# Kernel optimization log

Hardware: AMD Instinct MI355X
Metric: run time of the kernel (lower is better)

Reference implementation:

```python
import jax, jax.numpy as jnp
import numpy as np

N, E, B = 50000, 400000, 50
F_IN, HID, HEADS, F_OUT = 128, 32, 8, 64
HC = HID * HEADS  # 256


def gat_conv(x, src, dst, W, a_s, a_d, b, n):
    """PyG-style GATConv (concat=True, negative_slope=0.2), inference mode."""
    H, C = a_s.shape
    h = (x @ W).reshape(n, H, C)                       # [N,H,C]
    alpha_s = (h * a_s).sum(-1)                        # [N,H]
    alpha_d = (h * a_d).sum(-1)                        # [N,H]
    logits = jax.nn.leaky_relu(alpha_s[src] + alpha_d[dst], 0.2)  # [E,H]
    m = jax.ops.segment_max(logits, dst, num_segments=n)
    m = jnp.where(jnp.isfinite(m), m, 0.0)
    e = jnp.exp(logits - m[dst])
    den = jax.ops.segment_sum(e, dst, num_segments=n)
    alpha = e / (den[dst] + 1e-16)                     # segment softmax over dst
    out = jax.ops.segment_sum(h[src] * alpha[:, :, None], dst, num_segments=n)
    return out.reshape(n, H * C) + b


def setup_inputs() -> dict:
    key = jax.random.key(0)
    ks = jax.random.split(key, 24)
    s = 0.1
    inp = {
        "x": jax.random.normal(ks[0], (N, F_IN), jnp.float32),
        "edge_index": jax.random.randint(ks[1], (2, E), 0, N),
        "batch": jnp.sort(jax.random.randint(ks[2], (N,), 0, B)),
        "W1": jax.random.normal(ks[3], (F_IN, HC), jnp.float32) * s,
        "a_src1": jax.random.normal(ks[4], (HEADS, HID), jnp.float32) * s,
        "a_dst1": jax.random.normal(ks[5], (HEADS, HID), jnp.float32) * s,
        "b1": jnp.zeros((HC,), jnp.float32),
        "W2": jax.random.normal(ks[6], (HC, HC), jnp.float32) * s,
        "a_src2": jax.random.normal(ks[7], (1, HC), jnp.float32) * s,
        "a_dst2": jax.random.normal(ks[8], (1, HC), jnp.float32) * s,
        "b2": jnp.zeros((HC,), jnp.float32),
        "W3": jax.random.normal(ks[9], (HC, HC), jnp.float32) * s,
        "a_src3": jax.random.normal(ks[10], (1, HC), jnp.float32) * s,
        "a_dst3": jax.random.normal(ks[11], (1, HC), jnp.float32) * s,
        "b3": jnp.zeros((HC,), jnp.float32),
        "W4": jax.random.normal(ks[12], (HC, F_OUT), jnp.float32) * s,
        "a_src4": jax.random.normal(ks[13], (1, F_OUT), jnp.float32) * s,
        "a_dst4": jax.random.normal(ks[14], (1, F_OUT), jnp.float32) * s,
        "b4": jnp.zeros((F_OUT,), jnp.float32),
        "Wl": jax.random.normal(ks[15], (F_OUT, 1), jnp.float32) * s,
        "bl": jnp.zeros((1,), jnp.float32),
    }
    return inp


def reference(x, edge_index, batch, W1, a_src1, a_dst1, b1, W2, a_src2, a_dst2, b2,
              W3, a_src3, a_dst3, b3, W4, a_src4, a_dst4, b4, Wl, bl):
    n = x.shape[0]
    loop = jnp.arange(n)
    src = jnp.concatenate([edge_index[0], loop])  # add self loops (PyG default)
    dst = jnp.concatenate([edge_index[1], loop])
    x = jax.nn.elu(gat_conv(x, src, dst, W1, a_src1, a_dst1, b1, n))
    x = jax.nn.elu(gat_conv(x, src, dst, W2, a_src2, a_dst2, b2, n))
    x = jax.nn.elu(gat_conv(x, src, dst, W3, a_src3, a_dst3, b3, n))
    x_gat = gat_conv(x, src, dst, W4, a_src4, a_dst4, b4, n)
    # to_dense_batch(x_gat, batch).mean(dim=1): sum per graph / max graph size
    counts = jax.ops.segment_sum(jnp.ones((n,), x_gat.dtype), batch, num_segments=B)
    max_nodes = counts.max()
    pooled = jax.ops.segment_sum(x_gat, batch, num_segments=B) / max_nodes  # [B,F_OUT]
    return pooled @ Wl + bl  # [B,1]
```

## Files before the change

kernel.cpp:

```cpp
#include <hip/hip_runtime.h>
#include <math.h>


typedef __attribute__((ext_vector_type(8))) short short8;
typedef __attribute__((ext_vector_type(4))) float f32x4;

__device__ __forceinline__ unsigned short f2bf(float f) {
  unsigned int u = __builtin_bit_cast(unsigned int, f);
  unsigned int r = u + 0x7FFFu + ((u >> 16) & 1u);
  return (unsigned short)(r >> 16);
}
__device__ __forceinline__ float bf2f(unsigned short h) {
  unsigned int u = ((unsigned int)h) << 16;
  return __builtin_bit_cast(float, u);
}
__device__ __forceinline__ unsigned short f2h(float f) {
  _Float16 h = (_Float16)f;
  return __builtin_bit_cast(unsigned short, h);
}
__device__ __forceinline__ float h2f(unsigned short u) {
  return (float)__builtin_bit_cast(_Float16, u);
}

__device__ __forceinline__ void gload16(const unsigned short* g, unsigned short* l) {
  __builtin_amdgcn_global_load_lds(
      (const __attribute__((address_space(1))) void*)g,
      (__attribute__((address_space(3))) void*)l, 16, 0, 0);
}

template<int H>
__global__ __launch_bounds__(256) void k_gemm_mfma(
    const unsigned short* __restrict__ A2, const unsigned short* __restrict__ Wt,
    unsigned short* __restrict__ C, const float* __restrict__ avec_s,
    const float* __restrict__ avec_d, float* __restrict__ outS,
    float* __restrict__ outD, int M, int Kb, int Nc)
{
  __shared__ unsigned short lds[12288];
  unsigned short* As = lds;
  unsigned short* Bs = lds + 4096;
  const int tid = threadIdx.x;
  const int w = tid >> 6, l = tid & 63;
  const int row0 = blockIdx.x * 64, col0 = blockIdx.y * 128;
  const int wr = w >> 1, wc = w & 1;
  const int fr = l & 15, kg = l >> 4;
  const int xr = (fr & 7) << 4;
  const int sK = 2 * Kb;
  const int csrc = 8 * ((l & 7) ^ ((l >> 3) & 7));
  const int lrow = l >> 3;

  f32x4 acc[2][4];
  #pragma unroll
  for (int i = 0; i < 2; i++)
    #pragma unroll
    for (int j = 0; j < 4; j++) acc[i][j] = (f32x4){0.f, 0.f, 0.f, 0.f};

  for (int kp = 0; kp < sK; kp += 64) {
    #pragma unroll
    for (int i = 0; i < 2; i++) {
      int q = w * 2 + i;
      gload16(&A2[(size_t)(row0 + q * 8 + lrow) * sK + (kp + csrc)], &As[q * 512]);
    }
    #pragma unroll
    for (int i = 0; i < 4; i++) {
      int q = w * 4 + i;
      gload16(&Wt[(size_t)(col0 + q * 8 + lrow) * sK + (kp + csrc)], &Bs[q * 512]);
    }
    __syncthreads();
    #pragma unroll
    for (int kk = 0; kk < 2; kk++) {
      short8 a[2], b[4];
      #pragma unroll
      for (int mi = 0; mi < 2; mi++) {
        int r = wr * 32 + mi * 16 + fr;
        int off = r * 128 + ((kk * 64 + kg * 16) ^ xr);
        a[mi] = *(const short8*)((const char*)As + off);
      }
      #pragma unroll
      for (int ni = 0; ni < 4; ni++) {
        int c = wc * 64 + ni * 16 + fr;
        int off = c * 128 + ((kk * 64 + kg * 16) ^ xr);
        b[ni] = *(const short8*)((const char*)Bs + off);
      }
      #pragma unroll
      for (int mi = 0; mi < 2; mi++)
        #pragma unroll
        for (int ni = 0; ni < 4; ni++)
          acc[mi][ni] = __builtin_amdgcn_mfma_f32_16x16x32_bf16(
              a[mi], b[ni], acc[mi][ni], 0, 0, 0);
    }
    __syncthreads();
  }

  #pragma unroll
  for (int mi = 0; mi < 2; mi++)
    #pragma unroll
    for (int ni = 0; ni < 4; ni++)
      #pragma unroll
      for (int rr = 0; rr < 4; rr++) {
        int row = wr * 32 + mi * 16 + kg * 4 + rr;
        int c = wc * 64 + ni * 16 + fr;
        int sc = c ^ (((row >> 1) & 7) << 3);
        lds[row * 128 + sc] = f2h(acc[mi][ni][rr]);
      }
  __syncthreads();

  constexpr int RW = (H == 8) ? 4 : 16;
  const int Ch = Nc / H;
  const int rbase = tid >> 4;
  const int cc = tid & 15;
  const int c0 = cc * 8;
  const int gc0 = col0 + c0;
  float as8[8], ad8[8];
  #pragma unroll
  for (int j = 0; j < 8; j++) {
    bool ok = (gc0 + j) < Nc;
    as8[j] = ok ? avec_s[gc0 + j] : 0.f;
    ad8[j] = ok ? avec_d[gc0 + j] : 0.f;
  }
  #pragma unroll
  for (int i = 0; i < 4; i++) {
    int row = rbase + i * 16;
    int gr = row0 + row;
    int scc = c0 ^ (((row >> 1) & 7) << 3);
    short8 cv = *(const short8*)&lds[row * 128 + scc];
    if (gr < M && gc0 < Nc)
      *(short8*)&C[(size_t)gr * Nc + gc0] = cv;
    float ps = 0.f, pd = 0.f;
    #pragma unroll
    for (int j = 0; j < 8; j++) {
      float cf = h2f((unsigned short)cv[j]);
      ps = fmaf(cf, as8[j], ps);
      pd = fmaf(cf, ad8[j], pd);
    }
    #pragma unroll
    for (int off = 1; off < RW; off <<= 1) {
      ps += __shfl_xor(ps, off);
      pd += __shfl_xor(pd, off);
    }
    if ((tid & (RW - 1)) == 0 && gr < M) {
      int head = gc0 / Ch;
      atomicAdd(&outS[gr * H + head], ps);
      atomicAdd(&outD[gr * H + head], pd);
    }
  }
}

__global__ __launch_bounds__(256) void k_packX(const float* __restrict__ x,
    unsigned short* __restrict__ A2, int N, int Mpad)
{
  int row = blockIdx.x * 8 + (threadIdx.x >> 5);
  int c = (threadIdx.x & 31) * 4;
  if (row >= Mpad) return;
  float4 v = make_float4(0.f, 0.f, 0.f, 0.f);
  if (row < N) v = *(const float4*)&x[(size_t)row * 128 + c];
  float f[4] = {v.x, v.y, v.z, v.w};
  unsigned short hi[4], lo[4];
  #pragma unroll
  for (int i = 0; i < 4; i++) {
    hi[i] = f2bf(f[i]);
    lo[i] = f2bf(f[i] - bf2f(hi[i]));
  }
  size_t base = (size_t)row * 256 + c;
  *(uint2*)&A2[base] = make_uint2((unsigned)hi[0] | ((unsigned)hi[1] << 16),
                                  (unsigned)hi[2] | ((unsigned)hi[3] << 16));
  *(uint2*)&A2[base + 128] = make_uint2((unsigned)lo[0] | ((unsigned)lo[1] << 16),
                                        (unsigned)lo[2] | ((unsigned)lo[3] << 16));
}

__global__ void k_packW(const float* __restrict__ W, unsigned short* __restrict__ Wt,
                        int K, int NC, int NCPAD)
{
  int idx = blockIdx.x * 256 + threadIdx.x;
  int K2 = 2 * K;
  if (idx >= NCPAD * K2) return;
  int c = idx / K2, kp = idx % K2;
  unsigned short o = 0;
  if (c < NC) o = f2bf(W[(size_t)(kp % K) * NC + c]);
  Wt[(size_t)c * K2 + kp] = o;
}

template<int H>
__global__ void k_wcomp(const float* __restrict__ aS, const float* __restrict__ aD,
    const int* __restrict__ col, const int* __restrict__ rid,
    float* __restrict__ wbuf, int M)
{
  int idx = blockIdx.x * 256 + threadIdx.x;
  if (idx >= M) return;
  int e = idx / H, hd = idx % H;
  int s = col[e], r = rid[e];
  float lg = aS[s * H + hd] + aD[r * H + hd];
  lg = fmaxf(lg, 0.2f * lg);
  wbuf[idx] = __expf(lg);
}

template<int H, int HC, int ELU, int SPLIT>
__global__ __launch_bounds__(256) void k_aggregate(const unsigned short* __restrict__ h,
    const float* __restrict__ wbuf,
    const int* __restrict__ rowptr, const int* __restrict__ col,
    const float* __restrict__ bias, float* __restrict__ xout,
    unsigned short* __restrict__ a2out, int N)
{
  constexpr int VEC = HC / 64;
  constexpr int C = HC / H;
  constexpr int CH = (H == 8) ? 8 : 64;
  __shared__ float wlds[4][64];
  int wave = threadIdx.x >> 6, lane = threadIdx.x & 63;
  int row = blockIdx.x * 4 + wave;
  if (row >= N) return;
  const int cb = lane * VEC;
  const int hdg = cb / C;
  int s0 = rowptr[row], s1 = rowptr[row + 1];

  float den = 0.f;
  float acc[VEC];
  #pragma unroll
  for (int v = 0; v < VEC; v++) acc[v] = 0.f;

  for (int base = s0; base < s1; base += CH) {
    int cnt = min(CH, s1 - base);
    int eo = (H == 8) ? (lane >> 3) : lane;
    bool valid = eo < cnt;
    int s = col[valid ? (base + eo) : (s1 - 1)];
    float wv = valid ? wbuf[(size_t)base * H + lane] : 0.f;
    float d = wv;
    if constexpr (H == 8) {
      d += __shfl_xor(d, 8); d += __shfl_xor(d, 16); d += __shfl_xor(d, 32);
      wlds[wave][lane] = wv;
    } else {
      #pragma unroll
      for (int off = 1; off < 64; off <<= 1) d += __shfl_xor(d, off);
    }
    den += d;
    if (H == 8) {
      asm volatile("s_waitcnt lgkmcnt(0)" ::: "memory");
    }
    #pragma unroll 2
    for (int j = 0; j < cnt; j++) {
      int sj = __builtin_amdgcn_readlane(s, (H == 8) ? (j * 8) : j);
      float wj;
      if constexpr (H == 8) {
        wj = wlds[wave][j * 8 + hdg];
      } else {
        wj = __builtin_bit_cast(float,
              __builtin_amdgcn_readlane(__builtin_bit_cast(int, wv), j));
      }
      if constexpr (VEC == 4) {
        uint2 raw = *(const uint2*)&h[(size_t)sj * HC + cb];
        acc[0] = fmaf(wj, h2f((unsigned short)(raw.x & 0xFFFF)), acc[0]);
        acc[1] = fmaf(wj, h2f((unsigned short)(raw.x >> 16)),    acc[1]);
        acc[2] = fmaf(wj, h2f((unsigned short)(raw.y & 0xFFFF)), acc[2]);
        acc[3] = fmaf(wj, h2f((unsigned short)(raw.y >> 16)),    acc[3]);
      } else {
        acc[0] = fmaf(wj, h2f(h[(size_t)sj * HC + cb]), acc[0]);
      }
    }
  }
  if (H == 8) den = __shfl(den, hdg);
  float inv = 1.f / (den + 1e-16f);
  float o[VEC];
  #pragma unroll
  for (int v = 0; v < VEC; v++) {
    float t = acc[v] * inv + bias[cb + v];
    if (ELU) t = t > 0.f ? t : expm1f(t);
    o[v] = t;
  }
  if constexpr (SPLIT) {
    unsigned short hi[4], lo[4];
    #pragma unroll
    for (int v = 0; v < 4; v++) {
      hi[v] = f2bf(o[v]);
      lo[v] = f2bf(o[v] - bf2f(hi[v]));
    }
    size_t b2 = (size_t)row * (2 * HC) + cb;
    *(uint2*)&a2out[b2] = make_uint2((unsigned)hi[0] | ((unsigned)hi[1] << 16),
                                     (unsigned)hi[2] | ((unsigned)hi[3] << 16));
    *(uint2*)&a2out[b2 + HC] = make_uint2((unsigned)lo[0] | ((unsigned)lo[1] << 16),
                                          (unsigned)lo[2] | ((unsigned)lo[3] << 16));
  } else if constexpr (VEC == 4) {
    *(float4*)&xout[(size_t)row * HC + cb] = make_float4(o[0], o[1], o[2], o[3]);
  } else {
    xout[(size_t)row * HC + cb] = o[0];
  }
}

__global__ void k_init(int* deg, float* pool, unsigned short* A2, int N, int B,
                       int Mpad) {
  int i = blockIdx.x * 256 + threadIdx.x;
  if (i < N) deg[i] = 1;
  if (i < B * 64) pool[i] = 0.f;
  int padn = (Mpad - N) * 512;
  if (i < padn) A2[(size_t)N * 512 + i] = 0;
}

__global__ void k_deg(const int* __restrict__ ei, int* deg, int E) {
  int e = blockIdx.x * 256 + threadIdx.x;
  if (e < E) atomicAdd(&deg[ei[E + e]], 1);
}

__global__ void k_counts(const int* __restrict__ bat, int* cnt, int N, int B) {
  int b = threadIdx.x;
  if (b >= B) return;
  int lo0 = 0, hi0 = N;
  while (lo0 < hi0) { int mid = (lo0 + hi0) >> 1; if (bat[mid] < b) lo0 = mid + 1; else hi0 = mid; }
  int lo1 = lo0, hi1 = N;
  while (lo1 < hi1) { int mid = (lo1 + hi1) >> 1; if (bat[mid] < b + 1) lo1 = mid + 1; else hi1 = mid; }
  cnt[b] = lo1 - lo0;
}

__global__ __launch_bounds__(256) void k_scan1(const int* __restrict__ deg,
                                               int* csum, int N, int chunk) {
  int bid = blockIdx.x, t = threadIdx.x;
  int lo = bid * chunk, hi = min(lo + chunk, N);
  int s = 0;
  for (int i = lo + t; i < hi; i += 256) s += deg[i];
  #pragma unroll
  for (int off = 32; off; off >>= 1) s += __shfl_xor(s, off);
  __shared__ int sh[4];
  if ((t & 63) == 0) sh[t >> 6] = s;
  __syncthreads();
  if (t == 0) csum[bid] = sh[0] + sh[1] + sh[2] + sh[3];
}

__global__ __launch_bounds__(256) void k_scan2(const int* __restrict__ csum,
                                               int* coff) {
  __shared__ int s[256];
  int t = threadIdx.x;
  int v0 = csum[t];
  s[t] = v0;
  for (int off = 1; off < 256; off <<= 1) {
    __syncthreads();
    int v = (t >= off) ? s[t - off] : 0;
    __syncthreads();
    s[t] += v;
  }
  __syncthreads();
  coff[t] = s[t] - v0;
}

__global__ __launch_bounds__(256) void k_scan3(const int* __restrict__ deg,
    const int* __restrict__ coff, int* rowptr, int* cursor, int N, int chunk) {
  __shared__ int s[256];
  int bid = blockIdx.x, t = threadIdx.x;
  int i = bid * chunk + t;
  int v = (t < chunk && i < N) ? deg[i] : 0;
  s[t] = v;
  for (int off = 1; off < 256; off <<= 1) {
    __syncthreads();
    int x = (t >= off) ? s[t - off] : 0;
    __syncthreads();
    s[t] += x;
  }
  __syncthreads();
  int excl = s[t] - v + coff[bid];
  if (t < chunk && i < N) {
    rowptr[i] = excl;
    cursor[i] = excl;
    if (i == N - 1) rowptr[N] = excl + v;
  }
}

__global__ void k_scatter(const int* __restrict__ ei, int* cursor, int* col,
                          int* rid, int E, int N) {
  int idx = blockIdx.x * 256 + threadIdx.x;
  if (idx >= E + N) return;
  int s, d;
  if (idx < E) { s = ei[idx]; d = ei[E + idx]; }
  else         { s = d = idx - E; }
  int pos = atomicAdd(&cursor[d], 1);
  col[pos] = s;
  rid[pos] = d;
}

__global__ __launch_bounds__(256) void k_pool(const float* __restrict__ xg,
    const int* __restrict__ bat, float* pool, int N) {
  int lane = threadIdx.x & 63, w = threadIdx.x >> 6;
  int base = (blockIdx.x * 4 + w) * 16;
  if (base >= N) return;
  int end = min(base + 16, N);
  float local = 0.f;
  int curb = bat[base];
  for (int n = base; n < end; n++) {
    int b = bat[n];
    if (b != curb) {
      atomicAdd(&pool[curb * 64 + lane], local);
      local = 0.f; curb = b;
    }
    local += xg[(size_t)n * 64 + lane];
  }
  atomicAdd(&pool[curb * 64 + lane], local);
}

__global__ void k_final(const float* __restrict__ pool, const int* __restrict__ cnt,
    const float* __restrict__ Wl, const float* __restrict__ bl,
    float* __restrict__ out, int B) {
  int lane = threadIdx.x;
  int c = (lane < B) ? cnt[lane] : 0;
  #pragma unroll
  for (int off = 32; off; off >>= 1) c = max(c, __shfl_xor(c, off));
  float invm = 1.f / (float)c;
  float wl = Wl[lane];
  for (int b = 0; b < B; b++) {
    float ps = pool[b * 64 + lane] * wl;
    #pragma unroll
    for (int off = 32; off; off >>= 1) ps += __shfl_xor(ps, off);
    if (lane == 0) out[b] = ps * invm + bl[0];
  }
}

extern "C" void kernel_launch(void* const* d_in, const int* in_sizes, int n_in,
                              void* d_out, int out_size, void* d_ws, size_t ws_size,
                              hipStream_t stream)
{
  (void)n_in; (void)ws_size;
  const float* x   = (const float*)d_in[0];
  const int*   ei  = (const int*)d_in[1];
  const int*   bat = (const int*)d_in[2];
  const float* W1  = (const float*)d_in[3];
  const float* as1 = (const float*)d_in[4];
  const float* ad1 = (const float*)d_in[5];
  const float* b1  = (const float*)d_in[6];
  const float* W2  = (const float*)d_in[7];
  const float* as2 = (const float*)d_in[8];
  const float* ad2 = (const float*)d_in[9];
  const float* b2  = (const float*)d_in[10];
  const float* W3  = (const float*)d_in[11];
  const float* as3 = (const float*)d_in[12];
  const float* ad3 = (const float*)d_in[13];
  const float* b3  = (const float*)d_in[14];
  const float* W4  = (const float*)d_in[15];
  const float* as4 = (const float*)d_in[16];
  const float* ad4 = (const float*)d_in[17];
  const float* b4  = (const float*)d_in[18];
  const float* Wl  = (const float*)d_in[19];
  const float* bl  = (const float*)d_in[20];
  float* out = (float*)d_out;

  const int N = in_sizes[0] / 128;
  const int E = in_sizes[1] / 2;
  const int B = out_size;
  const int Mpad = ((N + 127) / 128) * 128;
  const int EN = E + N;

  char* p = (char*)d_ws;
  auto alloc = [&](size_t bytes) -> void* {
    void* r = (void*)p;
    p += ((bytes + 255) & ~(size_t)255);
    return r;
  };
  unsigned short* A2 = (unsigned short*)alloc((size_t)Mpad * 512 * 2);
  unsigned short* hbuf = (unsigned short*)alloc((size_t)N * 256 * 2);
  unsigned short* w2t1 = (unsigned short*)alloc((size_t)256 * 512 * 2);
  unsigned short* w2t2 = (unsigned short*)alloc((size_t)256 * 512 * 2);
  unsigned short* w2t3 = (unsigned short*)alloc((size_t)256 * 512 * 2);
  unsigned short* w2t4 = (unsigned short*)alloc((size_t)128 * 512 * 2);
  float* aAll  = (float*)alloc((size_t)N * 22 * 4);
  float* aSb   = aAll;
  float* aDb   = aAll + (size_t)N * 11;
  float* wbuf  = (float*)alloc((size_t)EN * 8 * 4);
  int*   deg   = (int*)alloc((size_t)N * 4);
  int*   rowptr= (int*)alloc((size_t)(N + 1) * 4);
  int*   cursor= (int*)alloc((size_t)N * 4);
  int*   col   = (int*)alloc((size_t)EN * 4);
  int*   rid   = (int*)alloc((size_t)EN * 4);
  int*   csum  = (int*)alloc(256 * 4);
  int*   coff  = (int*)alloc(256 * 4);
  float* pool  = (float*)alloc((size_t)B * 64 * 4);
  int*   cnt   = (int*)alloc((size_t)B * 4);
  float* xpool = (float*)A2;

  const int chunk = (N + 255) / 256;
  dim3 T(256);

  k_init<<<dim3((N + 255) / 256), T, 0, stream>>>(deg, pool, A2, N, B, Mpad);
  k_deg<<<dim3((E + 255) / 256), T, 0, stream>>>(ei, deg, E);
  k_counts<<<dim3(1), dim3(64), 0, stream>>>(bat, cnt, N, B);
  k_scan1<<<dim3(256), T, 0, stream>>>(deg, csum, N, chunk);
  k_scan2<<<dim3(1), T, 0, stream>>>(csum, coff);
  k_scan3<<<dim3(256), T, 0, stream>>>(deg, coff, rowptr, cursor, N, chunk);
  k_scatter<<<dim3((EN + 255) / 256), T, 0, stream>>>(ei, cursor, col, rid, E, N);
  hipMemsetAsync(aAll, 0, (size_t)N * 22 * 4, stream);

  k_packX<<<dim3(Mpad / 8), T, 0, stream>>>(x, A2, N, Mpad);
  k_packW<<<dim3((256 * 256 + 255) / 256), T, 0, stream>>>(W1, w2t1, 128, 256, 256);
  k_packW<<<dim3((256 * 512 + 255) / 256), T, 0, stream>>>(W2, w2t2, 256, 256, 256);
  k_packW<<<dim3((256 * 512 + 255) / 256), T, 0, stream>>>(W3, w2t3, 256, 256, 256);
  k_packW<<<dim3((128 * 512 + 255) / 256), T, 0, stream>>>(W4, w2t4, 256, 64, 128);

  dim3 nwav((N + 3) / 4);
  dim3 g2(Mpad / 64, 2), g1(Mpad / 64, 1);
  dim3 gw8((EN * 8 + 255) / 256), gw1((EN + 255) / 256);

  float* aS1 = aSb;                 float* aD1 = aDb;
  float* aS2 = aSb + (size_t)N * 8; float* aD2 = aDb + (size_t)N * 8;
  float* aS3 = aSb + (size_t)N * 9; float* aD3 = aDb + (size_t)N * 9;
  float* aS4 = aSb + (size_t)N * 10;float* aD4 = aDb + (size_t)N * 10;

  k_gemm_mfma<8><<<g2, T, 0, stream>>>(A2, w2t1, hbuf, as1, ad1, aS1, aD1, N, 128, 256);
  k_wcomp<8><<<gw8, T, 0, stream>>>(aS1, aD1, col, rid, wbuf, EN * 8);
  k_aggregate<8, 256, 1, 1><<<nwav, T, 0, stream>>>(hbuf, wbuf, rowptr, col, b1,
                                                    nullptr, A2, N);
  k_gemm_mfma<1><<<g2, T, 0, stream>>>(A2, w2t2, hbuf, as2, ad2, aS2, aD2, N, 256, 256);
  k_wcomp<1><<<gw1, T, 0, stream>>>(aS2, aD2, col, rid, wbuf, EN);
  k_aggregate<1, 256, 1, 1><<<nwav, T, 0, stream>>>(hbuf, wbuf, rowptr, col, b2,
                                                    nullptr, A2, N);
  k_gemm_mfma<1><<<g2, T, 0, stream>>>(A2, w2t3, hbuf, as3, ad3, aS3, aD3, N, 256, 256);
  k_wcomp<1><<<gw1, T, 0, stream>>>(aS3, aD3, col, rid, wbuf, EN);
  k_aggregate<1, 256, 1, 1><<<nwav, T, 0, stream>>>(hbuf, wbuf, rowptr, col, b3,
                                                    nullptr, A2, N);
  k_gemm_mfma<1><<<g1, T, 0, stream>>>(A2, w2t4, hbuf, as4, ad4, aS4, aD4, N, 256, 64);
  k_wcomp<1><<<gw1, T, 0, stream>>>(aS4, aD4, col, rid, wbuf, EN);
  k_aggregate<1, 64, 0, 0><<<nwav, T, 0, stream>>>(hbuf, wbuf, rowptr, col, b4,
                                                   xpool, nullptr, N);

  k_pool<<<dim3((N + 63) / 64), T, 0, stream>>>(xpool, bat, pool, N);
  k_final<<<dim3(1), dim3(64), 0, stream>>>(pool, cnt, Wl, bl, out, B);
}
```

Measured before the change: 462.9 us.

## Merge weight-pack and count launches, use fma_mix in aggregation, widen unroll

Merges the four weight-packing kernels into a single launch and folds the per-graph count binary search into the scan2 kernel, removing several small launches. In the aggregation inner loop, the half-to-float conversion plus fma is replaced with v_fma_mix_f32 inline asm, 32-bit offsets are used, and the unroll factor goes from 2 to 4. The aim is less launch overhead and fewer ALU and address instructions in the gather loop. The risk is higher register pressure from the wider unroll, and inline asm limits compiler scheduling.

```diff
diff --git a/kernel.cpp b/kernel.cpp
--- a/kernel.cpp
+++ b/kernel.cpp
@@ -20,6 +20,15 @@
 }
 __device__ __forceinline__ float h2f(unsigned short u) {
   return (float)__builtin_bit_cast(_Float16, u);
+}
+
+__device__ __forceinline__ void fma_mix_lo(float& acc, unsigned int packed, float w) {
+  asm("v_fma_mix_f32 %0, %1, %2, %0 op_sel_hi:[1,0,0]"
+      : "+v"(acc) : "v"(packed), "v"(w));
+}
+__device__ __forceinline__ void fma_mix_hi(float& acc, unsigned int packed, float w) {
+  asm("v_fma_mix_f32 %0, %1, %2, %0 op_sel:[1,0,0] op_sel_hi:[1,0,0]"
+      : "+v"(acc) : "v"(packed), "v"(w));
 }
 
 __device__ __forceinline__ void gload16(const unsigned short* g, unsigned short* l) {
@@ -167,16 +176,26 @@
                                         (unsigned)lo[2] | ((unsigned)lo[3] << 16));
 }
 
-__global__ void k_packW(const float* __restrict__ W, unsigned short* __restrict__ Wt,
-                        int K, int NC, int NCPAD)
-{
-  int idx = blockIdx.x * 256 + threadIdx.x;
+__device__ __forceinline__ void packW_one(const float* __restrict__ W,
+    unsigned short* __restrict__ Wt, int K, int NC, int idx)
+{
   int K2 = 2 * K;
-  if (idx >= NCPAD * K2) return;
   int c = idx / K2, kp = idx % K2;
   unsigned short o = 0;
   if (c < NC) o = f2bf(W[(size_t)(kp % K) * NC + c]);
   Wt[(size_t)c * K2 + kp] = o;
+}
+
+__global__ void k_packW_all(const float* __restrict__ W1, const float* __restrict__ W2,
+    const float* __restrict__ W3, const float* __restrict__ W4,
+    unsigned short* __restrict__ t1, unsigned short* __restrict__ t2,
+    unsigned short* __restrict__ t3, unsigned short* __restrict__ t4)
+{
+  int idx = blockIdx.x * 256 + threadIdx.x;
+  if (idx < 65536)            packW_one(W1, t1, 128, 256, idx);
+  else if (idx < 196608)      packW_one(W2, t2, 256, 256, idx - 65536);
+  else if (idx < 327680)      packW_one(W3, t3, 256, 256, idx - 196608);
+  else if (idx < 393216)      packW_one(W4, t4, 256,  64, idx - 327680);
 }
 
 template<int H>
@@ -221,7 +240,7 @@
     int eo = (H == 8) ? (lane >> 3) : lane;
     bool valid = eo < cnt;
     int s = col[valid ? (base + eo) : (s1 - 1)];
-    float wv = valid ? wbuf[(size_t)base * H + lane] : 0.f;
+    float wv = valid ? wbuf[(unsigned)(base * H) + lane] : 0.f;
     float d = wv;
     if constexpr (H == 8) {
       d += __shfl_xor(d, 8); d += __shfl_xor(d, 16); d += __shfl_xor(d, 32);
@@ -234,7 +253,7 @@
     if (H == 8) {
       asm volatile("s_waitcnt lgkmcnt(0)" ::: "memory");
     }
-    #pragma unroll 2
+    #pragma unroll 4
     for (int j = 0; j < cnt; j++) {
       int sj = __builtin_amdgcn_readlane(s, (H == 8) ? (j * 8) : j);
       float wj;
@@ -244,14 +263,16 @@
         wj = __builtin_bit_cast(float,
               __builtin_amdgcn_readlane(__builtin_bit_cast(int, wv), j));
       }
+      unsigned off = (unsigned)sj * HC + cb;
       if constexpr (VEC == 4) {
-        uint2 raw = *(const uint2*)&h[(size_t)sj * HC + cb];
-        acc[0] = fmaf(wj, h2f((unsigned short)(raw.x & 0xFFFF)), acc[0]);
-        acc[1] = fmaf(wj, h2f((unsigned short)(raw.x >> 16)),    acc[1]);
-        acc[2] = fmaf(wj, h2f((unsigned short)(raw.y & 0xFFFF)), acc[2]);
-        acc[3] = fmaf(wj, h2f((unsigned short)(raw.y >> 16)),    acc[3]);
+        uint2 raw = *(const uint2*)(h + off);
+        fma_mix_lo(acc[0], raw.x, wj);
+        fma_mix_hi(acc[1], raw.x, wj);
+        fma_mix_lo(acc[2], raw.y, wj);
+        fma_mix_hi(acc[3], raw.y, wj);
       } else {
-        acc[0] = fmaf(wj, h2f(h[(size_t)sj * HC + cb]), acc[0]);
+        unsigned int raw = h[off];
+        fma_mix_lo(acc[0], raw, wj);
       }
     }
   }
@@ -297,16 +318,6 @@
   if (e < E) atomicAdd(&deg[ei[E + e]], 1);
 }
 
-__global__ void k_counts(const int* __restrict__ bat, int* cnt, int N, int B) {
-  int b = threadIdx.x;
-  if (b >= B) return;
-  int lo0 = 0, hi0 = N;
-  while (lo0 < hi0) { int mid = (lo0 + hi0) >> 1; if (bat[mid] < b) lo0 = mid + 1; else hi0 = mid; }
-  int lo1 = lo0, hi1 = N;
-  while (lo1 < hi1) { int mid = (lo1 + hi1) >> 1; if (bat[mid] < b + 1) lo1 = mid + 1; else hi1 = mid; }
-  cnt[b] = lo1 - lo0;
-}
-
 __global__ __launch_bounds__(256) void k_scan1(const int* __restrict__ deg,
                                                int* csum, int N, int chunk) {
   int bid = blockIdx.x, t = threadIdx.x;
@@ -322,7 +333,7 @@
 }
 
 __global__ __launch_bounds__(256) void k_scan2(const int* __restrict__ csum,
-                                               int* coff) {
+    int* coff, const int* __restrict__ bat, int* cnt, int N, int B) {
   __shared__ int s[256];
   int t = threadIdx.x;
   int v0 = csum[t];
@@ -335,6 +346,13 @@
   }
   __syncthreads();
   coff[t] = s[t] - v0;
+  if (t < B) {
+    int lo0 = 0, hi0 = N;
+    while (lo0 < hi0) { int mid = (lo0 + hi0) >> 1; if (bat[mid] < t) lo0 = mid + 1; else hi0 = mid; }
+    int lo1 = lo0, hi1 = N;
+    while (lo1 < hi1) { int mid = (lo1 + hi1) >> 1; if (bat[mid] < t + 1) lo1 = mid + 1; else hi1 = mid; }
+    cnt[t] = lo1 - lo0;
+  }
 }
 
 __global__ __launch_bounds__(256) void k_scan3(const int* __restrict__ deg,
@@ -473,18 +491,14 @@
 
   k_init<<<dim3((N + 255) / 256), T, 0, stream>>>(deg, pool, A2, N, B, Mpad);
   k_deg<<<dim3((E + 255) / 256), T, 0, stream>>>(ei, deg, E);
-  k_counts<<<dim3(1), dim3(64), 0, stream>>>(bat, cnt, N, B);
   k_scan1<<<dim3(256), T, 0, stream>>>(deg, csum, N, chunk);
-  k_scan2<<<dim3(1), T, 0, stream>>>(csum, coff);
+  k_scan2<<<dim3(1), T, 0, stream>>>(csum, coff, bat, cnt, N, B);
   k_scan3<<<dim3(256), T, 0, stream>>>(deg, coff, rowptr, cursor, N, chunk);
   k_scatter<<<dim3((EN + 255) / 256), T, 0, stream>>>(ei, cursor, col, rid, E, N);
   hipMemsetAsync(aAll, 0, (size_t)N * 22 * 4, stream);
 
   k_packX<<<dim3(Mpad / 8), T, 0, stream>>>(x, A2, N, Mpad);
-  k_packW<<<dim3((256 * 256 + 255) / 256), T, 0, stream>>>(W1, w2t1, 128, 256, 256);
-  k_packW<<<dim3((256 * 512 + 255) / 256), T, 0, stream>>>(W2, w2t2, 256, 256, 256);
-  k_packW<<<dim3((256 * 512 + 255) / 256), T, 0, stream>>>(W3, w2t3, 256, 256, 256);
-  k_packW<<<dim3((128 * 512 + 255) / 256), T, 0, stream>>>(W4, w2t4, 256, 64, 128);
+  k_packW_all<<<dim3(1536), T, 0, stream>>>(W1, W2, W3, W4, w2t1, w2t2, w2t3, w2t4);
 
   dim3 nwav((N + 3) / 4);
   dim3 g2(Mpad / 64, 2), g1(Mpad / 64, 1);
```

After: 461.1 us. About the same (-0.4%).
